# Optimization experiments

Measured on AMD Instinct MI355X. Metric: run time of the kernel, lower is better.

The kernel has to match this reference:

```python
import jax, jax.numpy as jnp
import numpy as np

T, B = 512, 256
OBS, FEAT, H, ACT = 128, 512, 256, 16
LOG2PI = float(np.log(2.0 * np.pi))


def layer_norm(x, w, b, eps=1e-5):
    m = x.mean(-1, keepdims=True)
    v = ((x - m) ** 2).mean(-1, keepdims=True)
    return (x - m) / jnp.sqrt(v + eps) * w + b


def mlp_features(x, W1, b1, W2, b2, gw, gb):
    h = jax.nn.relu(x @ W1.T + b1)
    h = layer_norm(h @ W2.T + b2, gw, gb)
    return jax.nn.relu(h)


def masked_lstm_scan(feat, done, h0, c0, Wih, Whh, bih, bhh):
    # feat: [T,B,H], done: [T,B] float, h0/c0: [B,H]. PyTorch gate order i,f,g,o.
    def step(carry, inp):
        h, c = carry
        x, d = inp
        m = (1.0 - d)[:, None]
        h = h * m
        c = c * m
        g = x @ Wih.T + bih + h @ Whh.T + bhh
        i, f, gg, o = jnp.split(g, 4, axis=-1)
        c = jax.nn.sigmoid(f) * c + jax.nn.sigmoid(i) * jnp.tanh(gg)
        h = jax.nn.sigmoid(o) * jnp.tanh(c)
        return (h, c), h
    (hT, cT), hs = jax.lax.scan(step, (h0, c0), (feat, done))
    return hs, hT, cT


def setup_inputs():
    key = jax.random.key(0)
    ks = jax.random.split(key, 40)
    rn = lambda k, s, sc=0.05: jax.random.normal(k, s, dtype=jnp.float32) * sc
    inp = {}
    inp["x"] = jax.random.normal(ks[0], (T * B, OBS), dtype=jnp.float32)
    inp["done"] = jax.random.randint(ks[1], (T * B,), 0, 2).astype(jnp.int32)
    inp["actor_h0"] = rn(ks[2], (1, B, H), 0.1)
    inp["actor_c0"] = rn(ks[3], (1, B, H), 0.1)
    inp["critic_h0"] = rn(ks[4], (1, B, H), 0.1)
    inp["critic_c0"] = rn(ks[5], (1, B, H), 0.1)
    inp["action"] = jax.random.normal(ks[6], (T * B, ACT), dtype=jnp.float32)
    j = 7
    for p in ("a", "c"):
        inp[p + "_W1"] = rn(ks[j], (FEAT, OBS)); j += 1
        inp[p + "_b1"] = jnp.zeros((FEAT,), jnp.float32)
        inp[p + "_W2"] = rn(ks[j], (H, FEAT)); j += 1
        inp[p + "_b2"] = jnp.zeros((H,), jnp.float32)
        inp[p + "_flnw"] = jnp.ones((H,), jnp.float32)
        inp[p + "_flnb"] = jnp.zeros((H,), jnp.float32)
        inp[p + "_Wih"] = rn(ks[j], (4 * H, H)); j += 1
        inp[p + "_Whh"] = rn(ks[j], (4 * H, H)); j += 1
        inp[p + "_bih"] = jnp.zeros((4 * H,), jnp.float32)
        inp[p + "_bhh"] = jnp.zeros((4 * H,), jnp.float32)
        inp[p + "_lnw"] = jnp.ones((H,), jnp.float32)
        inp[p + "_lnb"] = jnp.zeros((H,), jnp.float32)
    inp["a_mW"] = rn(ks[j], (ACT, H)); j += 1
    inp["a_mb"] = jnp.zeros((ACT,), jnp.float32)
    inp["a_logstd"] = jnp.zeros((1, ACT), jnp.float32)
    inp["c_hW"] = rn(ks[j], (1, H)); j += 1
    inp["c_hb"] = jnp.zeros((1,), jnp.float32)
    return inp


def reference(x, done, actor_h0, actor_c0, critic_h0, critic_c0, action,
              a_W1, a_b1, a_W2, a_b2, a_flnw, a_flnb, a_Wih, a_Whh, a_bih, a_bhh,
              a_lnw, a_lnb, a_mW, a_mb, a_logstd,
              c_W1, c_b1, c_W2, c_b2, c_flnw, c_flnb, c_Wih, c_Whh, c_bih, c_bhh,
              c_lnw, c_lnb, c_hW, c_hb):
    Bn = actor_h0.shape[1]
    N = x.shape[0]
    Tn = N // Bn
    d = done.astype(jnp.float32).reshape(Tn, Bn)
    # actor branch
    a_feat = mlp_features(x, a_W1, a_b1, a_W2, a_b2, a_flnw, a_flnb).reshape(Tn, Bn, -1)
    hs, ah, acell = masked_lstm_scan(a_feat, d, actor_h0[0], actor_c0[0], a_Wih, a_Whh, a_bih, a_bhh)
    ha = layer_norm(hs.reshape(N, -1), a_lnw, a_lnb)
    mean = ha @ a_mW.T + a_mb
    logstd = jnp.broadcast_to(a_logstd, mean.shape)
    std = jnp.exp(logstd)
    logprob = (-0.5 * ((action - mean) / std) ** 2 - logstd - 0.5 * LOG2PI).sum(1)
    entropy = (0.5 + 0.5 * LOG2PI + logstd).sum(1)
    # critic branch
    c_feat = mlp_features(x, c_W1, c_b1, c_W2, c_b2, c_flnw, c_flnb).reshape(Tn, Bn, -1)
    cs, ch, ccell = masked_lstm_scan(c_feat, d, critic_h0[0], critic_c0[0], c_Wih, c_Whh, c_bih, c_bhh)
    hc = layer_norm(cs.reshape(N, -1), c_lnw, c_lnb)
    value = hc @ c_hW.T + c_hb
    return (logprob, entropy, value, ah[None], acell[None], ch[None], ccell[None])
```

## Files before the change

kernel.cpp:

```cpp
#include <hip/hip_runtime.h>

typedef unsigned short u16;
typedef unsigned long long u64;
typedef __attribute__((ext_vector_type(8))) short short8;
typedef __attribute__((ext_vector_type(4))) float floatx4;
typedef __attribute__((ext_vector_type(4))) float f32x4;
typedef __attribute__((ext_vector_type(4))) int intx4;

#define LOG2PI_F 1.8378770664093453f
#define LOG2E_F 1.4426950408889634f
#define TWOLOG2E_F 2.8853900817779268f

__device__ inline float bf2f(u16 u) { return __uint_as_float(((unsigned)u) << 16); }
__device__ inline u16 f2bf(float f) {
  unsigned u = __float_as_uint(f);
  u += 0x7fff + ((u >> 16) & 1);
  return (u16)(u >> 16);
}

struct PrepArgs {
  const float* src[18];
  const float* src2[18];
  void* dst[18];
  int mode[18];
  int n[18];
  int blk0[19];
  int nseg;
};

__global__ __launch_bounds__(256) void k_prep(PrepArgs a) {
  int b = blockIdx.x, s = 0;
  while (s + 1 < a.nseg && b >= a.blk0[s + 1]) ++s;
  int i = (b - a.blk0[s]) * 1024 + threadIdx.x * 4;
  if (i >= a.n[s]) return;
  if (a.mode[s] == 0) {
    f32x4 v = *(const f32x4*)(a.src[s] + i);
    u64 p = (u64)f2bf(v[0]) | ((u64)f2bf(v[1]) << 16)
          | ((u64)f2bf(v[2]) << 32) | ((u64)f2bf(v[3]) << 48);
    *(u64*)((u16*)a.dst[s] + i) = p;
  } else if (a.mode[s] == 1) {
    f32x4 x = *(const f32x4*)(a.src[s] + i);
    f32x4 y = *(const f32x4*)(a.src2[s] + i);
    *(f32x4*)((float*)a.dst[s] + i) = x + y;
  } else {
    *(f32x4*)((float*)a.dst[s] + i) = *(const f32x4*)(a.src[s] + i);
  }
}

__global__ __launch_bounds__(256) void k_quant(const float* __restrict__ w0,
                                               const float* __restrict__ w1,
                                               char* __restrict__ q, float* __restrict__ sr) {
  int tid = threadIdx.x, lane = tid & 63;
  int row = blockIdx.x * 4 + (tid >> 6);
  int br = row >> 10, r = row & 1023;
  const float* src = (br ? w1 : w0) + (size_t)r * 256 + lane * 4;
  f32x4 v = *(const f32x4*)src;
  float m = fmaxf(fmaxf(fabsf(v[0]), fabsf(v[1])), fmaxf(fabsf(v[2]), fabsf(v[3])));
#pragma unroll
  for (int o = 32; o >= 1; o >>= 1) m = fmaxf(m, __shfl_xor(m, o));
  float inv = m > 0.f ? 127.f / m : 0.f;
  int pk = 0;
#pragma unroll
  for (int c = 0; c < 4; ++c) {
    int qq = __float2int_rn(v[c] * inv);
    qq = qq > 127 ? 127 : (qq < -127 ? -127 : qq);
    pk |= (qq & 255) << (8 * c);
  }
  *(int*)(q + (size_t)row * 256 + lane * 4) = pk;
  if (lane == 0) {
    float sf = (r >= 512 && r < 768) ? TWOLOG2E_F : -LOG2E_F;
    sr[row] = m * (1.f / (127.f * 127.f)) * sf;
  }
}

template <int EPI, int AF32>
__global__ __launch_bounds__(256, 2) void k_gemm(
    const void* __restrict__ Agv, const u16* __restrict__ Wg,
    const float* __restrict__ biasP, void* __restrict__ outv,
    int Nn, int K, int relu, int Tseg,
    long az, long wz, long oz) {
  __shared__ u16 As[128][72];
  __shared__ u16 Ws[128][72];
  const int tid = threadIdx.x;
  const int z = blockIdx.z;
  const int bn = blockIdx.x * 128;
  const int bm = blockIdx.y * 128;
  const int w = tid >> 6, lane = tid & 63, lm = lane & 15, lq = lane >> 4;
  const int wr = (w >> 1) * 64, wc = (w & 1) * 64;
  const int tr = tid >> 3, tc = (tid & 7) * 8;

  const u16* Ab = (const u16*)Agv;
  const float* Af = (const float*)Agv;
  const u16* Wb = Wg + (size_t)z * wz;

  floatx4 acc[4][4] = {};

  for (int k0 = 0; k0 < K; k0 += 64) {
    __syncthreads();
#pragma unroll
    for (int rr = 0; rr < 4; ++rr) {
      int row = rr * 32 + tr;
      if (AF32) {
        const float* src = Af + (size_t)z * az + (size_t)(bm + row) * K + k0 + tc;
        f32x4 v0 = *(const f32x4*)src;
        f32x4 v1 = *(const f32x4*)(src + 4);
        short8 sv;
#pragma unroll
        for (int c = 0; c < 4; ++c) { sv[c] = (short)f2bf(v0[c]); sv[4 + c] = (short)f2bf(v1[c]); }
        *(short8*)&As[row][tc] = sv;
      } else {
        *(short8*)&As[row][tc] = *(const short8*)(Ab + (size_t)z * az + (size_t)(bm + row) * K + k0 + tc);
      }
      *(short8*)&Ws[row][tc] = *(const short8*)(Wb + (size_t)(bn + row) * K + k0 + tc);
    }
    __syncthreads();
#pragma unroll
    for (int kk = 0; kk < 2; ++kk) {
      short8 a4[4], b4[4];
#pragma unroll
      for (int i = 0; i < 4; ++i) {
        a4[i] = *(const short8*)&As[wr + i * 16 + lm][kk * 32 + lq * 8];
        b4[i] = *(const short8*)&Ws[wc + i * 16 + lm][kk * 32 + lq * 8];
      }
#pragma unroll
      for (int i = 0; i < 4; ++i)
#pragma unroll
        for (int j = 0; j < 4; ++j)
          acc[i][j] = __builtin_amdgcn_mfma_f32_16x16x32_bf16(a4[i], b4[j], acc[i][j], 0, 0, 0);
    }
  }

#pragma unroll
  for (int i = 0; i < 4; ++i) {
#pragma unroll
    for (int j = 0; j < 4; ++j) {
      int col = bn + wc + j * 16 + lm;
      float bv = biasP[(size_t)z * Nn + col];
      float v[4];
#pragma unroll
      for (int r = 0; r < 4; ++r) {
        float t = acc[i][j][r] + bv;
        v[r] = relu ? fmaxf(t, 0.f) : t;
      }
      int row0l = bm + wr + i * 16 + lq * 4;
      if (EPI == 1) {
        u16* o = (u16*)outv + (size_t)z * oz;
#pragma unroll
        for (int r = 0; r < 4; ++r) o[(size_t)(row0l + r) * Nn + col] = f2bf(v[r]);
      } else {
        float s = (col >= 512 && col < 768) ? TWOLOG2E_F : -LOG2E_F;
        int t_l = row0l >> 8;
        int bfull = row0l & 255;
        int bbx = bfull >> 4;
        int mq = (bfull >> 2) & 3;
        u64 p = (u64)f2bf(v[0] * s) | ((u64)f2bf(v[1] * s) << 16)
              | ((u64)f2bf(v[2] * s) << 32) | ((u64)f2bf(v[3] * s) << 48);
        u16* o = (u16*)outv + (size_t)z * oz;
        size_t idx = ((((size_t)bbx * Tseg + t_l) * 4 + mq) * 1024 + col) * 4;
        *(u64*)(o + idx) = p;
      }
    }
  }
}

__global__ __launch_bounds__(256) void k_ln_relu(const u16* __restrict__ in,
                                                 const float* __restrict__ lnp,
                                                 u16* __restrict__ out,
                                                 long inz, long outz) {
  int z = blockIdx.y;
  int w = threadIdx.x >> 6, lane = threadIdx.x & 63;
  size_t row = (size_t)blockIdx.x * 4 + w;
  const u16* ip = in + (size_t)z * inz;
  u16* op = out + (size_t)z * outz;
  const float* gw = lnp + (size_t)z * 512;
  const float* gb = gw + 256;
  u64 hv = *(const u64*)(ip + row * 256 + lane * 4);
  float x[4];
#pragma unroll
  for (int c = 0; c < 4; ++c) x[c] = bf2f((u16)(hv >> (16 * c)));
  float s = x[0] + x[1] + x[2] + x[3];
  float q = x[0] * x[0] + x[1] * x[1] + x[2] * x[2] + x[3] * x[3];
#pragma unroll
  for (int o = 32; o >= 1; o >>= 1) { s += __shfl_xor(s, o); q += __shfl_xor(q, o); }
  float mean = s * (1.f / 256.f);
  float var = q * (1.f / 256.f) - mean * mean;
  float rs = rsqrtf(var + 1e-5f);
  u64 p = 0;
#pragma unroll
  for (int c = 0; c < 4; ++c) {
    int k = lane * 4 + c;
    float y = (x[c] - mean) * rs * gw[k] + gb[k];
    y = fmaxf(y, 0.f);
    p |= ((u64)f2bf(y)) << (16 * c);
  }
  *(u64*)(op + row * 256 + lane * 4) = p;
}

struct ScanArgs {
  const u16 *gin0, *gin1;
  const char *whq0, *whq1;
  const float *sr0, *sr1;
  const float *h00, *h01, *c00, *c01;
  char *hs0, *hs1;
  float *hsv0, *hsv1, *csv0, *csv1;
  const int* done;
  int t0, Tseg;
};

__global__ __launch_bounds__(512, 2) void k_scan(ScanArgs A) {
  const int bb = blockIdx.x & 31, br = blockIdx.x >> 5;
  const int bbx = bb >> 1, half = bb & 1;
  const int rb = bb << 3;
  const int tid = threadIdx.x;
  const int w = tid >> 6, lane = tid & 63, lm = lane & 15, lq = lane >> 4;
  const int u = lq >> 1;
  const int jj = (w + 8 * u) * 16 + lm;
  const int rlo = (lq & 1) * 4;
  const int wj = w + 8 * u;
  const int hoff = (wj >> 2) * 1024 + ((wj & 3) * 16 + rlo) * 16 + lm;

  extern __shared__ char dsm[];
  char* hl = dsm;

  const char* whq = br ? A.whq1 : A.whq0;
  const float* srP = br ? A.sr1 : A.sr0;
  const u16* gin = (br ? A.gin1 : A.gin0) + (size_t)bbx * A.Tseg * 16384;
  const float* h0 = br ? A.h01 : A.h00;
  const float* c0 = br ? A.c01 : A.c00;
  char* hs = (br ? A.hs1 : A.hs0) + bbx * 4096;
  float* hsv = br ? A.hsv1 : A.hsv0;
  float* csv = br ? A.csv1 : A.csv0;

  intx4 wreg[8][4];
#pragma unroll
  for (int a = 0; a < 8; ++a)
#pragma unroll
    for (int kk = 0; kk < 4; ++kk)
      wreg[a][kk] = *(const intx4*)(whq + (size_t)((w + 8 * a) * 16 + lm) * 256 + kk * 64 + lq * 16);

  float srw[4];
#pragma unroll
  for (int g = 0; g < 4; ++g) srw[g] = srP[g * 256 + jj];

  float creg[4];
#pragma unroll
  for (int r = 0; r < 4; ++r)
    creg[r] = c0[(size_t)(rb + rlo + r) * 256 + jj];

  {
    int c = tid & 255, buf = tid >> 8;
    int kk = c >> 6, lqk = (c >> 4) & 3, m = c & 15;
    intx4 val = {0, 0, 0, 0};
    if (buf == 0 && m < 8) {
      const float* hp = h0 + (size_t)(rb + m) * 256 + kk * 64 + lqk * 16;
#pragma unroll
      for (int q4 = 0; q4 < 4; ++q4) {
        int pk = 0;
#pragma unroll
        for (int b = 0; b < 4; ++b) {
          int qv = __float2int_rn(hp[q4 * 4 + b] * 127.f);
          qv = qv > 127 ? 127 : (qv < -127 ? -127 : qv);
          pk |= (qv & 255) << (8 * b);
        }
        val[q4] = pk;
      }
    }
    *(intx4*)&hl[buf * 4096 + c * 16] = val;
  }
  __syncthreads();

  const int mq = half * 2 + (lq & 1);
  u64 gnxt[4];
#pragma unroll
  for (int g = 0; g < 4; ++g)
    gnxt[g] = *(const u64*)(gin + ((size_t)mq * 1024 + g * 256 + jj) * 4);
  int daN = A.done[(size_t)A.t0 * 256 + rb + (lm & 7)];
  intx4 dcN = *(const intx4*)(A.done + (size_t)A.t0 * 256 + rb + rlo);

  intx4 z4 = {0, 0, 0, 0};

  for (int tl = 0; tl < A.Tseg; ++tl) {
    const int curo = (tl & 1) * 4096, nxto = curo ^ 4096;

    u64 gcur[4];
#pragma unroll
    for (int g = 0; g < 4; ++g) gcur[g] = gnxt[g];
    int da = daN;
    intx4 dc = dcN;

    if (tl + 1 < A.Tseg) {
#pragma unroll
      for (int g = 0; g < 4; ++g)
        gnxt[g] = *(const u64*)(gin + (((size_t)(tl + 1) * 4 + mq) * 1024 + g * 256 + jj) * 4);
      int tn = A.t0 + tl + 1;
      daN = A.done[(size_t)tn * 256 + rb + (lm & 7)];
      dcN = *(const intx4*)(A.done + (size_t)tn * 256 + rb + rlo);
    }

    intx4 af[4];
#pragma unroll
    for (int kk = 0; kk < 4; ++kk) {
      intx4 hv = *(const intx4*)&hl[curo + kk * 1024 + lane * 16];
      af[kk] = da ? z4 : hv;
    }

    intx4 acc[8] = {};
#pragma unroll
    for (int kk = 0; kk < 4; ++kk)
#pragma unroll
      for (int a = 0; a < 8; ++a)
        acc[a] = __builtin_amdgcn_mfma_i32_16x16x64_i8(af[kk], wreg[a][kk], acc[a], 0, 0, 0);

    float av[4][4];
#pragma unroll
    for (int g = 0; g < 4; ++g)
#pragma unroll
      for (int r = 0; r < 4; ++r) {
        int oth = __shfl_xor(acc[2 * g + 1][r], 32);
        av[g][r] = (float)(lq < 2 ? acc[2 * g][r] : oth);
      }

    floatx4 gf[4];
#pragma unroll
    for (int g = 0; g < 4; ++g) {
      u64 gv = gcur[g];
      floatx4 v;
      v[0] = bf2f((u16)gv); v[1] = bf2f((u16)(gv >> 16));
      v[2] = bf2f((u16)(gv >> 32)); v[3] = bf2f((u16)(gv >> 48));
      gf[g] = v;
    }

#pragma unroll
    for (int r = 0; r < 4; ++r) {
      float cprev = dc[r] ? 0.f : creg[r];
      float xi = fmaf(av[0][r], srw[0], gf[0][r]);
      float xf = fmaf(av[1][r], srw[1], gf[1][r]);
      float xg = fmaf(av[2][r], srw[2], gf[2][r]);
      float xo = fmaf(av[3][r], srw[3], gf[3][r]);
      float ig = __builtin_amdgcn_rcpf(1.f + __builtin_amdgcn_exp2f(xi));
      float fg = __builtin_amdgcn_rcpf(1.f + __builtin_amdgcn_exp2f(xf));
      float gg = 1.f - 2.f * __builtin_amdgcn_rcpf(1.f + __builtin_amdgcn_exp2f(xg));
      float og = __builtin_amdgcn_rcpf(1.f + __builtin_amdgcn_exp2f(xo));
      float cn = fg * cprev + ig * gg;
      creg[r] = cn;
      float th = 1.f - 2.f * __builtin_amdgcn_rcpf(1.f + __builtin_amdgcn_exp2f(TWOLOG2E_F * cn));
      float hn = og * th;
      int qv = __float2int_rn(hn * 127.f);
      hl[nxto + hoff + r * 16] = (char)qv;
      if (tl == A.Tseg - 1) {
        size_t idx = (size_t)(rb + rlo + r) * 256 + jj;
        hsv[idx] = hn;
        csv[idx] = cn;
      }
    }
    asm volatile("s_waitcnt lgkmcnt(0)" ::: "memory");
    __builtin_amdgcn_s_barrier();
    __builtin_amdgcn_sched_barrier(0);
    {
      int idx = tid * 4;
      int kk2 = idx >> 9, i2 = idx & 511;
      int lqk2 = i2 >> 7, m2 = (i2 >> 4) & 7, b2 = i2 & 15;
      int lo = nxto + kk2 * 1024 + lqk2 * 256 + m2 * 16 + b2;
      int go = kk2 * 1024 + lqk2 * 256 + half * 128 + m2 * 16 + b2;
      *(int*)(hs + (size_t)tl * 65536 + go) = *(const int*)&hl[lo];
    }
  }
}

__global__ __launch_bounds__(256) void k_head(
    const char* __restrict__ hs_a, const char* __restrict__ hs_c,
    const float* __restrict__ a_lnw, const float* __restrict__ a_lnb,
    const float* __restrict__ c_lnw, const float* __restrict__ c_lnb,
    const float* __restrict__ mW, const float* __restrict__ mb,
    const float* __restrict__ logstd, const float* __restrict__ hW,
    const float* __restrict__ hb, const float* __restrict__ action,
    float* __restrict__ lp, float* __restrict__ ent, float* __restrict__ val,
    int row0) {
  __shared__ float smW[16][260];
  __shared__ float shW[256];
  __shared__ float spar[4][256];
  __shared__ float hrow[4][264];
  int tid = threadIdx.x;
  for (int i = tid; i < 4096; i += 256) smW[i >> 8][i & 255] = mW[i];
  shW[tid] = hW[tid];
  spar[0][tid] = a_lnw[tid]; spar[1][tid] = a_lnb[tid];
  spar[2][tid] = c_lnw[tid]; spar[3][tid] = c_lnb[tid];
  __syncthreads();

  int w = tid >> 6, lane = tid & 63, lm = lane & 15, lq = lane >> 4;
  float entc = 0.f;
#pragma unroll
  for (int j = 0; j < 16; ++j) entc += 0.5f + 0.5f * LOG2PI_F + logstd[j];
  float ls = logstd[lm];
  float sd = __expf(ls);
  float mbj = mb[lm];

  int rbase = (blockIdx.x * 4 + w) * 16;
  for (int rr = 0; rr < 16; ++rr) {
    int row = rbase + rr;
    int m = row & 15;
    size_t base = (size_t)(row >> 8) * 65536 + (size_t)((row >> 4) & 15) * 4096;
    int off = (lane >> 4) * 1024 + (m + 16 * ((lane >> 2) & 3)) * 16 + (lane & 3) * 4;
    int va = *(const int*)(hs_a + base + off);
    float x[4];
#pragma unroll
    for (int c = 0; c < 4; ++c) x[c] = (float)((va << (24 - 8 * c)) >> 24) * (1.f / 127.f);
    float s = x[0] + x[1] + x[2] + x[3];
    float q = x[0] * x[0] + x[1] * x[1] + x[2] * x[2] + x[3] * x[3];
#pragma unroll
    for (int o = 32; o >= 1; o >>= 1) { s += __shfl_xor(s, o); q += __shfl_xor(q, o); }
    float mean = s * (1.f / 256.f);
    float rs = rsqrtf(q * (1.f / 256.f) - mean * mean + 1e-5f);
    floatx4 hh;
#pragma unroll
    for (int c = 0; c < 4; ++c) {
      int k = lane * 4 + c;
      hh[c] = (x[c] - mean) * rs * spar[0][k] + spar[1][k];
    }
    *(floatx4*)&hrow[w][lane * 4] = hh;
    float p = 0.f;
#pragma unroll 16
    for (int k2 = 0; k2 < 64; ++k2) {
      int kx = lq * 64 + ((k2 + lq * 16) & 63);
      p = fmaf(hrow[w][kx], smW[lm][kx], p);
    }
    p += __shfl_xor(p, 16);
    p += __shfl_xor(p, 32);
    float meanj = p + mbj;
    float aj = action[(size_t)(row0 + row) * 16 + lm];
    float z = (aj - meanj) / sd;
    float term = -0.5f * z * z - ls - 0.5f * LOG2PI_F;
    term += __shfl_xor(term, 1);
    term += __shfl_xor(term, 2);
    term += __shfl_xor(term, 4);
    term += __shfl_xor(term, 8);
    int vc = *(const int*)(hs_c + base + off);
    float y[4];
#pragma unroll
    for (int c = 0; c < 4; ++c) y[c] = (float)((vc << (24 - 8 * c)) >> 24) * (1.f / 127.f);
    float s2 = y[0] + y[1] + y[2] + y[3];
    float q2 = y[0] * y[0] + y[1] * y[1] + y[2] * y[2] + y[3] * y[3];
#pragma unroll
    for (int o = 32; o >= 1; o >>= 1) { s2 += __shfl_xor(s2, o); q2 += __shfl_xor(q2, o); }
    float mean2 = s2 * (1.f / 256.f);
    float rs2 = rsqrtf(q2 * (1.f / 256.f) - mean2 * mean2 + 1e-5f);
    float pv = 0.f;
#pragma unroll
    for (int c = 0; c < 4; ++c) {
      int k = lane * 4 + c;
      float hc = (y[c] - mean2) * rs2 * spar[2][k] + spar[3][k];
      pv = fmaf(hc, shW[k], pv);
    }
#pragma unroll
    for (int o = 32; o >= 1; o >>= 1) pv += __shfl_xor(pv, o);
    if (lane == 0) {
      lp[row0 + row] = term;
      ent[row0 + row] = entc;
      val[row0 + row] = pv + hb[0];
    }
  }
}

extern "C" void kernel_launch(void* const* d_in, const int* in_sizes, int n_in,
                              void* d_out, int out_size, void* d_ws, size_t ws_size,
                              hipStream_t stream) {
  const int N = 131072, T = 512;
  const float* x = (const float*)d_in[0];
  const int* done = (const int*)d_in[1];
  const float* h0i[2] = {(const float*)d_in[2], (const float*)d_in[4]};
  const float* c0i[2] = {(const float*)d_in[3], (const float*)d_in[5]};
  const float* action = (const float*)d_in[6];
  const float *W1[2], *b1[2], *W2[2], *b2[2], *flnw[2], *flnb[2];
  const float *Wih[2], *Whh[2], *bih[2], *bhh[2], *lnw[2], *lnb[2];
  for (int br = 0; br < 2; ++br) {
    int o = 7 + br * 12;
    W1[br] = (const float*)d_in[o + 0];  b1[br] = (const float*)d_in[o + 1];
    W2[br] = (const float*)d_in[o + 2];  b2[br] = (const float*)d_in[o + 3];
    flnw[br] = (const float*)d_in[o + 4]; flnb[br] = (const float*)d_in[o + 5];
    Wih[br] = (const float*)d_in[o + 6]; Whh[br] = (const float*)d_in[o + 7];
    bih[br] = (const float*)d_in[o + 8]; bhh[br] = (const float*)d_in[o + 9];
    lnw[br] = (const float*)d_in[o + 10]; lnb[br] = (const float*)d_in[o + 11];
  }
  const float* mW = (const float*)d_in[31];
  const float* mb = (const float*)d_in[32];
  const float* logstd = (const float*)d_in[33];
  const float* hW = (const float*)d_in[34];
  const float* hb = (const float*)d_in[35];

  float* out = (float*)d_out;
  float* o_lp = out;
  float* o_ent = out + N;
  float* o_val = out + 2 * N;
  float* o_ah = out + 3 * N;
  float* o_ac = o_ah + 65536;
  float* o_ch = o_ac + 65536;
  float* o_cc = o_ch + 65536;

  auto rq = [&](long sr2, long st2) -> size_t {
    long Ts = T / st2, Ms = N / sr2;
    size_t s = 0;
    auto al = [&](size_t b) { s += (b + 255) & ~(size_t)255; };
    al(2 * 65536 * 2); al(2 * 131072 * 2); al(2 * 262144 * 2);
    al(2 * 262144); al(2048 * 4);
    al(2 * 1024 * 4); al(2 * 512 * 4); al(2 * 256 * 4); al(1024 * 4);
    al(2 * 65536 * 4); al(2 * 65536 * 4);
    al((size_t)2 * Ms * 512 * 2);
    al((size_t)2 * Ms * 256 * 2);
    al((size_t)2 * N * 256 * 2);
    al((size_t)2 * Ts * 262144 * 2);
    al((size_t)2 * Ts * 65536);
    return s;
  };
  int sr = 16, st = 16;
  const int cand[7][2] = {{1, 1}, {2, 2}, {4, 4}, {4, 8}, {8, 8}, {8, 16}, {16, 16}};
  for (int i = 0; i < 7; ++i)
    if (rq(cand[i][0], cand[i][1]) + ((size_t)4 << 20) <= ws_size) { sr = cand[i][0]; st = cand[i][1]; break; }
  const long Ts = T / st, Ms = N / sr;

  char* pp = (char*)d_ws;
  auto carve = [&](size_t b) -> void* { void* r = pp; pp += (b + 255) & ~(size_t)255; return r; };
  u16* W1b = (u16*)carve(2 * 65536 * 2);
  u16* W2b = (u16*)carve(2 * 131072 * 2);
  u16* Wihb = (u16*)carve(2 * 262144 * 2);
  char* whhq = (char*)carve(2 * 262144);
  float* srowP = (float*)carve(2048 * 4);
  float* bihh = (float*)carve(2 * 1024 * 4);
  float* b1c = (float*)carve(2 * 512 * 4);
  float* b2c = (float*)carve(2 * 256 * 4);
  float* lnp = (float*)carve(1024 * 4);
  float* hsv = (float*)carve(2 * 65536 * 4);
  float* csv = (float*)carve(2 * 65536 * 4);
  u16* h1 = (u16*)carve((size_t)2 * Ms * 512 * 2);
  u16* g2 = (u16*)carve((size_t)2 * Ms * 256 * 2);
  u16* featP = (u16*)carve((size_t)2 * N * 256 * 2);
  u16* ginP = (u16*)carve((size_t)2 * Ts * 262144 * 2);
  char* hsbP = (char*)carve((size_t)2 * Ts * 65536);

  PrepArgs pa{};
  int ns = 0, blk = 0;
  auto addseg = [&](const float* s1, const float* s2, void* d, int n, int mode) {
    pa.src[ns] = s1; pa.src2[ns] = s2; pa.dst[ns] = d; pa.mode[ns] = mode; pa.n[ns] = n;
    pa.blk0[ns] = blk; blk += (n + 1023) / 1024; ++ns;
  };
  for (int br = 0; br < 2; ++br) {
    addseg(W1[br], nullptr, W1b + br * 65536, 65536, 0);
    addseg(W2[br], nullptr, W2b + br * 131072, 131072, 0);
    addseg(Wih[br], nullptr, Wihb + br * 262144, 262144, 0);
    addseg(bih[br], bhh[br], bihh + br * 1024, 1024, 1);
    addseg(b1[br], nullptr, b1c + br * 512, 512, 2);
    addseg(b2[br], nullptr, b2c + br * 256, 256, 2);
    addseg(flnw[br], nullptr, lnp + br * 512, 256, 2);
    addseg(flnb[br], nullptr, lnp + br * 512 + 256, 256, 2);
  }
  pa.nseg = ns;
  pa.blk0[ns] = blk;
  k_prep<<<blk, 256, 0, stream>>>(pa);
  k_quant<<<512, 256, 0, stream>>>(Whh[0], Whh[1], whhq, srowP);

  for (int s = 0; s < sr; ++s) {
    k_gemm<1, 1><<<dim3(4, Ms / 128, 2), 256, 0, stream>>>(
        x + (size_t)s * Ms * 128, W1b, b1c, h1, 512, 128, 1, 0,
        0L, 65536L, (long)Ms * 512);
    k_gemm<1, 0><<<dim3(2, Ms / 128, 2), 256, 0, stream>>>(
        h1, W2b, b2c, g2, 256, 512, 0, 0,
        (long)Ms * 512, 131072L, (long)Ms * 256);
    k_ln_relu<<<dim3(Ms / 4, 2), 256, 0, stream>>>(
        g2, lnp, featP + (size_t)s * Ms * 256, (long)Ms * 256, (long)N * 256);
  }

  for (int s = 0; s < st; ++s) {
    long t0 = s * Ts;
    k_gemm<2, 0><<<dim3(8, Ts * 2, 2), 256, 0, stream>>>(
        featP + (size_t)t0 * 65536, Wihb, bihh, ginP, 1024, 256, 0, (int)Ts,
        (long)N * 256, 262144L, Ts * 262144L);
    ScanArgs sa;
    sa.gin0 = ginP; sa.gin1 = ginP + Ts * 262144;
    sa.whq0 = whhq; sa.whq1 = whhq + 262144;
    sa.sr0 = srowP; sa.sr1 = srowP + 1024;
    sa.h00 = s ? hsv : h0i[0]; sa.h01 = s ? hsv + 65536 : h0i[1];
    sa.c00 = s ? csv : c0i[0]; sa.c01 = s ? csv + 65536 : c0i[1];
    sa.hs0 = hsbP; sa.hs1 = hsbP + Ts * 65536;
    bool last = (s == st - 1);
    sa.hsv0 = last ? o_ah : hsv; sa.hsv1 = last ? o_ch : hsv + 65536;
    sa.csv0 = last ? o_ac : csv; sa.csv1 = last ? o_cc : csv + 65536;
    sa.done = done; sa.t0 = (int)t0; sa.Tseg = (int)Ts;
    k_scan<<<64, 512, 8192, stream>>>(sa);
    k_head<<<(int)(Ts * 256 / 64), 256, 0, stream>>>(
        hsbP, hsbP + Ts * 65536, lnw[0], lnb[0], lnw[1], lnb[1],
        mW, mb, logstd, hW, hb, action,
        o_lp, o_ent, o_val, (int)(t0 * 256));
  }
}
```

Measured before the change: 2.078 ms.

## Split LSTM scan across 256 blocks with two batch rows each

The recurrent scan kernel now gives each block 2 batch rows instead of 8, so the grid grows from 64 to 256 blocks and uses more compute units. Each thread now handles one (row, hidden unit) cell. MFMA outputs are redistributed with lane shuffles, and the gate preactivation loads become scalar bf16 loads. The cost is that each MFMA tile is mostly padding and every block reloads the full recurrent weight matrix into registers.

```diff
diff --git a/kernel.cpp b/kernel.cpp
--- a/kernel.cpp
+++ b/kernel.cpp
@@ -208,16 +208,15 @@
 };
 
 __global__ __launch_bounds__(512, 2) void k_scan(ScanArgs A) {
-  const int bb = blockIdx.x & 31, br = blockIdx.x >> 5;
-  const int bbx = bb >> 1, half = bb & 1;
-  const int rb = bb << 3;
+  const int bb = blockIdx.x & 127, br = blockIdx.x >> 7;
+  const int bbx = bb >> 3;
+  const int rb = bb << 1;
   const int tid = threadIdx.x;
   const int w = tid >> 6, lane = tid & 63, lm = lane & 15, lq = lane >> 4;
-  const int u = lq >> 1;
-  const int jj = (w + 8 * u) * 16 + lm;
-  const int rlo = (lq & 1) * 4;
-  const int wj = w + 8 * u;
-  const int hoff = (wj >> 2) * 1024 + ((wj & 3) * 16 + rlo) * 16 + lm;
+  const int bsel = lq & 1;
+  const int mrow = lane >> 5;
+  const int jj = w * 32 + bsel * 16 + lm;
+  const int hoff = (jj >> 4) * 256 + mrow * 16 + (jj & 15);
 
   extern __shared__ char dsm[];
   char* hl = dsm;
@@ -233,25 +232,25 @@
 
   intx4 wreg[8][4];
 #pragma unroll
-  for (int a = 0; a < 8; ++a)
-#pragma unroll
-    for (int kk = 0; kk < 4; ++kk)
-      wreg[a][kk] = *(const intx4*)(whq + (size_t)((w + 8 * a) * 16 + lm) * 256 + kk * 64 + lq * 16);
+  for (int g = 0; g < 4; ++g)
+#pragma unroll
+    for (int b2 = 0; b2 < 2; ++b2)
+#pragma unroll
+      for (int kk = 0; kk < 4; ++kk)
+        wreg[g * 2 + b2][kk] =
+            *(const intx4*)(whq + (size_t)(g * 256 + w * 32 + b2 * 16 + lm) * 256 + kk * 64 + lq * 16);
 
   float srw[4];
 #pragma unroll
   for (int g = 0; g < 4; ++g) srw[g] = srP[g * 256 + jj];
 
-  float creg[4];
-#pragma unroll
-  for (int r = 0; r < 4; ++r)
-    creg[r] = c0[(size_t)(rb + rlo + r) * 256 + jj];
+  float creg = c0[(size_t)(rb + mrow) * 256 + jj];
 
   {
     int c = tid & 255, buf = tid >> 8;
     int kk = c >> 6, lqk = (c >> 4) & 3, m = c & 15;
     intx4 val = {0, 0, 0, 0};
-    if (buf == 0 && m < 8) {
+    if (buf == 0 && m < 2) {
       const float* hp = h0 + (size_t)(rb + m) * 256 + kk * 64 + lqk * 16;
 #pragma unroll
       for (int q4 = 0; q4 < 4; ++q4) {
@@ -269,32 +268,33 @@
   }
   __syncthreads();
 
-  const int mq = half * 2 + (lq & 1);
-  u64 gnxt[4];
+  const int goff = ((rb >> 2) & 3) * 4096 + (rb & 3) + mrow;
+
+  u16 gnxt[4];
 #pragma unroll
   for (int g = 0; g < 4; ++g)
-    gnxt[g] = *(const u64*)(gin + ((size_t)mq * 1024 + g * 256 + jj) * 4);
-  int daN = A.done[(size_t)A.t0 * 256 + rb + (lm & 7)];
-  intx4 dcN = *(const intx4*)(A.done + (size_t)A.t0 * 256 + rb + rlo);
+    gnxt[g] = gin[(size_t)(g * 256 + jj) * 4 + goff];
+  int daN = A.done[(size_t)A.t0 * 256 + rb + (lm & 1)];
+  int dcN = A.done[(size_t)A.t0 * 256 + rb + mrow];
 
   intx4 z4 = {0, 0, 0, 0};
 
   for (int tl = 0; tl < A.Tseg; ++tl) {
     const int curo = (tl & 1) * 4096, nxto = curo ^ 4096;
 
-    u64 gcur[4];
+    u16 gcur[4];
 #pragma unroll
     for (int g = 0; g < 4; ++g) gcur[g] = gnxt[g];
     int da = daN;
-    intx4 dc = dcN;
+    int dc = dcN;
 
     if (tl + 1 < A.Tseg) {
 #pragma unroll
       for (int g = 0; g < 4; ++g)
-        gnxt[g] = *(const u64*)(gin + (((size_t)(tl + 1) * 4 + mq) * 1024 + g * 256 + jj) * 4);
+        gnxt[g] = gin[(size_t)(tl + 1) * 16384 + (size_t)(g * 256 + jj) * 4 + goff];
       int tn = A.t0 + tl + 1;
-      daN = A.done[(size_t)tn * 256 + rb + (lm & 7)];
-      dcN = *(const intx4*)(A.done + (size_t)tn * 256 + rb + rlo);
+      daN = A.done[(size_t)tn * 256 + rb + (lm & 1)];
+      dcN = A.done[(size_t)tn * 256 + rb + mrow];
     }
 
     intx4 af[4];
@@ -311,44 +311,35 @@
       for (int a = 0; a < 8; ++a)
         acc[a] = __builtin_amdgcn_mfma_i32_16x16x64_i8(af[kk], wreg[a][kk], acc[a], 0, 0, 0);
 
-    float av[4][4];
-#pragma unroll
-    for (int g = 0; g < 4; ++g)
-#pragma unroll
-      for (int r = 0; r < 4; ++r) {
-        int oth = __shfl_xor(acc[2 * g + 1][r], 32);
-        av[g][r] = (float)(lq < 2 ? acc[2 * g][r] : oth);
-      }
-
-    floatx4 gf[4];
+    float av[4];
 #pragma unroll
     for (int g = 0; g < 4; ++g) {
-      u64 gv = gcur[g];
-      floatx4 v;
-      v[0] = bf2f((u16)gv); v[1] = bf2f((u16)(gv >> 16));
-      v[2] = bf2f((u16)(gv >> 32)); v[3] = bf2f((u16)(gv >> 48));
-      gf[g] = v;
-    }
-
-#pragma unroll
-    for (int r = 0; r < 4; ++r) {
-      float cprev = dc[r] ? 0.f : creg[r];
-      float xi = fmaf(av[0][r], srw[0], gf[0][r]);
-      float xf = fmaf(av[1][r], srw[1], gf[1][r]);
-      float xg = fmaf(av[2][r], srw[2], gf[2][r]);
-      float xo = fmaf(av[3][r], srw[3], gf[3][r]);
+      int s00 = __shfl(acc[2 * g][0], lm);
+      int s01 = __shfl(acc[2 * g][1], lm);
+      int s10 = __shfl(acc[2 * g + 1][0], lm);
+      int s11 = __shfl(acc[2 * g + 1][1], lm);
+      int sel = bsel ? (mrow ? s11 : s10) : (mrow ? s01 : s00);
+      av[g] = (float)sel;
+    }
+
+    {
+      float cprev = dc ? 0.f : creg;
+      float xi = fmaf(av[0], srw[0], bf2f(gcur[0]));
+      float xf = fmaf(av[1], srw[1], bf2f(gcur[1]));
+      float xg = fmaf(av[2], srw[2], bf2f(gcur[2]));
+      float xo = fmaf(av[3], srw[3], bf2f(gcur[3]));
       float ig = __builtin_amdgcn_rcpf(1.f + __builtin_amdgcn_exp2f(xi));
       float fg = __builtin_amdgcn_rcpf(1.f + __builtin_amdgcn_exp2f(xf));
       float gg = 1.f - 2.f * __builtin_amdgcn_rcpf(1.f + __builtin_amdgcn_exp2f(xg));
       float og = __builtin_amdgcn_rcpf(1.f + __builtin_amdgcn_exp2f(xo));
       float cn = fg * cprev + ig * gg;
-      creg[r] = cn;
+      creg = cn;
       float th = 1.f - 2.f * __builtin_amdgcn_rcpf(1.f + __builtin_amdgcn_exp2f(TWOLOG2E_F * cn));
       float hn = og * th;
       int qv = __float2int_rn(hn * 127.f);
-      hl[nxto + hoff + r * 16] = (char)qv;
+      hl[nxto + hoff] = (char)qv;
       if (tl == A.Tseg - 1) {
-        size_t idx = (size_t)(rb + rlo + r) * 256 + jj;
+        size_t idx = (size_t)(rb + mrow) * 256 + jj;
         hsv[idx] = hn;
         csv[idx] = cn;
       }
@@ -356,13 +347,11 @@
     asm volatile("s_waitcnt lgkmcnt(0)" ::: "memory");
     __builtin_amdgcn_s_barrier();
     __builtin_amdgcn_sched_barrier(0);
-    {
-      int idx = tid * 4;
-      int kk2 = idx >> 9, i2 = idx & 511;
-      int lqk2 = i2 >> 7, m2 = (i2 >> 4) & 7, b2 = i2 & 15;
-      int lo = nxto + kk2 * 1024 + lqk2 * 256 + m2 * 16 + b2;
-      int go = kk2 * 1024 + lqk2 * 256 + half * 128 + m2 * 16 + b2;
-      *(int*)(hs + (size_t)tl * 65536 + go) = *(const int*)&hl[lo];
+    if (tid < 128) {
+      int a_l = nxto + (tid >> 3) * 256 + (tid & 7) * 4;
+      int mg = (bb & 7) * 2 + ((tid >> 2) & 1);
+      int a_g = (tid >> 3) * 256 + mg * 16 + (tid & 3) * 4;
+      *(int*)(hs + (size_t)tl * 65536 + a_g) = *(const int*)&hl[a_l];
     }
   }
 }
@@ -584,7 +573,7 @@
     sa.hsv0 = last ? o_ah : hsv; sa.hsv1 = last ? o_ch : hsv + 65536;
     sa.csv0 = last ? o_ac : csv; sa.csv1 = last ? o_cc : csv + 65536;
     sa.done = done; sa.t0 = (int)t0; sa.Tseg = (int)Ts;
-    k_scan<<<64, 512, 8192, stream>>>(sa);
+    k_scan<<<256, 512, 8192, stream>>>(sa);
     k_head<<<(int)(Ts * 256 / 64), 256, 0, stream>>>(
         hsbP, hsbP + Ts * 65536, lnw[0], lnb[0], lnw[1], lnb[1],
         mW, mb, logstd, hW, hb, action,
```

After: 1.931 ms. 1.08x faster.
